# Kernel tuning notes

Measured on AMD Instinct MI355X. Metric: run time of the kernel, lower is better.

## Reference

```python
import jax, jax.numpy as jnp
import numpy as np

N_NODES = 100000
N_EDGES = 1600000
N_REL = 8
IN_CH = 64
HIDDEN = 64
OUT_CH = 32


def setup_inputs() -> dict:
    key = jax.random.key(0)
    ks = jax.random.split(key, 10)
    s_in = 1.0 / np.sqrt(IN_CH)
    s_h = 1.0 / np.sqrt(HIDDEN)
    return {
        "x": jax.random.normal(ks[0], (N_NODES, IN_CH), dtype=jnp.float32),
        "edge_index": jax.random.randint(ks[1], (2, N_EDGES), 0, N_NODES, dtype=jnp.int64),
        "edge_type": jax.random.randint(ks[2], (N_EDGES,), 0, N_REL, dtype=jnp.int64),
        "W0": jax.random.normal(ks[3], (N_REL, IN_CH, HIDDEN), dtype=jnp.float32) * s_in,
        "Q0": jax.random.normal(ks[4], (HIDDEN, 1), dtype=jnp.float32) * s_h,
        "K0": jax.random.normal(ks[5], (HIDDEN, 1), dtype=jnp.float32) * s_h,
        "b0": jnp.zeros((HIDDEN,), dtype=jnp.float32),
        "W1": jax.random.normal(ks[6], (N_REL, HIDDEN, OUT_CH), dtype=jnp.float32) * s_h,
        "Q1": jax.random.normal(ks[7], (OUT_CH, 1), dtype=jnp.float32) * (1.0 / np.sqrt(OUT_CH)),
        "K1": jax.random.normal(ks[8], (OUT_CH, 1), dtype=jnp.float32) * (1.0 / np.sqrt(OUT_CH)),
        "b1": jnp.zeros((OUT_CH,), dtype=jnp.float32),
    }


def rgat_conv(x, src, dst, et, W, Q, K, b, n_nodes):
    # relation-typed transform of all nodes: [R, N, out]
    xw = jnp.einsum("ni,rio->rno", x, W)
    # per-node, per-relation attention logits (heads=1, dim=1)
    q = jnp.einsum("rno,od->rnd", xw, Q)[..., 0]  # [R, N]
    k = jnp.einsum("rno,od->rnd", xw, K)[..., 0]  # [R, N]
    # additive self-attention, leaky_relu slope 0.2 (PyG RGATConv default)
    alpha = jax.nn.leaky_relu(q[et, dst] + k[et, src], negative_slope=0.2)  # [E]
    # across-relation segment softmax over incoming edges of each dst node
    amax = jax.ops.segment_max(alpha, dst, num_segments=n_nodes)
    a = jnp.exp(alpha - amax[dst])
    denom = jax.ops.segment_sum(a, dst, num_segments=n_nodes)
    a = a / (denom[dst] + 1e-16)
    # weighted scatter-add aggregation of transformed source features
    msg = a[:, None] * xw[et, src]  # [E, out]
    return jax.ops.segment_sum(msg, dst, num_segments=n_nodes) + b


def reference(x, edge_index, edge_type, W0, Q0, K0, b0, W1, Q1, K1, b1):
    src, dst = edge_index[0], edge_index[1]
    n = x.shape[0]
    h = rgat_conv(x, src, dst, edge_type, W0, Q0, K0, b0, n)
    h = jax.nn.relu(h)  # dropout p=0.0 -> identity
    out = rgat_conv(h, src, dst, edge_type, W1, Q1, K1, b1, n)
    return out
```

## Files before the change

### kernel.cpp

```cpp
#include <hip/hip_runtime.h>
#include <hip/hip_bf16.h>
#include <math.h>


#define CSR_CHUNK 8192

__global__ void k_bhist(const int* __restrict__ dst, int* __restrict__ bcount,
                        int E, int NB) {
    __shared__ int h[512];
    int t = threadIdx.x;
    for (int i = t; i < NB; i += 256) h[i] = 0;
    __syncthreads();
    int e0 = blockIdx.x * CSR_CHUNK;
    int e1 = min(e0 + CSR_CHUNK, E);
    for (int i = e0 + t; i < e1; i += 256) atomicAdd(&h[dst[i] >> 8], 1);
    __syncthreads();
    for (int i = t; i < NB; i += 256) {
        int c = h[i];
        if (c) atomicAdd(&bcount[i], c);
    }
}

__global__ void k_bscan(const int* __restrict__ bcount, int* __restrict__ bstart,
                        int* __restrict__ gcur, int* __restrict__ rowptr,
                        int NB, int N, int E) {
    __shared__ int s[512];
    int t = threadIdx.x;
    int v = (t < NB) ? bcount[t] : 0;
    s[t] = v;
    __syncthreads();
    for (int off = 1; off < 512; off <<= 1) {
        int a = (t >= off) ? s[t - off] : 0;
        __syncthreads();
        s[t] += a;
        __syncthreads();
    }
    int excl = s[t] - v;
    if (t < NB) {
        bstart[t] = excl;
        gcur[t] = excl;
    }
    if (t == 0) {
        bstart[NB] = E;
        rowptr[N] = E;
    }
}

__global__ void k_bscatter(const int* __restrict__ src, const int* __restrict__ dst,
                           const int* __restrict__ et, int* __restrict__ gcur,
                           unsigned* __restrict__ ebuf, int E, int NB) {
    __shared__ int h[512];
    __shared__ int basearr[512];
    int t = threadIdx.x;
    for (int i = t; i < NB; i += 256) h[i] = 0;
    __syncthreads();
    int e0 = blockIdx.x * CSR_CHUNK;
    int e1 = min(e0 + CSR_CHUNK, E);
    for (int i = e0 + t; i < e1; i += 256) atomicAdd(&h[dst[i] >> 8], 1);
    __syncthreads();
    for (int i = t; i < NB; i += 256) {
        int c = h[i];
        basearr[i] = c ? atomicAdd(&gcur[i], c) : 0;
        h[i] = 0;
    }
    __syncthreads();
    for (int i = e0 + t; i < e1; i += 256) {
        int d = dst[i];
        int b = d >> 8;
        int off = atomicAdd(&h[b], 1);
        ebuf[basearr[b] + off] =
            ((unsigned)(d & 255) << 20) | ((unsigned)et[i] << 17) | (unsigned)src[i];
    }
}

__global__ void k_bsort(const unsigned* __restrict__ ebuf, const int* __restrict__ bstart,
                        int* __restrict__ rowptr, int* __restrict__ csr, int N) {
    __shared__ int lh[2048];
    __shared__ int ls[2048];
    __shared__ int ss[256];
    int b = blockIdx.x, t = threadIdx.x;
    int e0 = bstart[b], e1 = bstart[b + 1];
    for (int i = t; i < 2048; i += 256) lh[i] = 0;
    __syncthreads();
    for (int i = e0 + t; i < e1; i += 256) {
        unsigned u = ebuf[i];
        atomicAdd(&lh[(int)(((u >> 20) & 255) * 8 + ((u >> 17) & 7))], 1);
    }
    __syncthreads();
    int loc[8];
    int s = 0;
#pragma unroll
    for (int j = 0; j < 8; j++) {
        loc[j] = s;
        s += lh[t * 8 + j];
    }
    ss[t] = s;
    __syncthreads();
    for (int off = 1; off < 256; off <<= 1) {
        int a = (t >= off) ? ss[t - off] : 0;
        __syncthreads();
        ss[t] += a;
        __syncthreads();
    }
    int excl = ss[t] - s;
#pragma unroll
    for (int j = 0; j < 8; j++) ls[t * 8 + j] = excl + loc[j];
    int node = b * 256 + t;
    if (node < N) rowptr[node] = e0 + excl;
    __syncthreads();
    for (int i = t; i < 2048; i += 256) lh[i] = 0;
    __syncthreads();
    for (int i = e0 + t; i < e1; i += 256) {
        unsigned u = ebuf[i];
        int key = (int)(((u >> 20) & 255) * 8 + ((u >> 17) & 7));
        int off = atomicAdd(&lh[key], 1);
        csr[e0 + ls[key] + off] = (int)(u & 0xFFFFF);
    }
}


__global__ void k_wt2(const float* __restrict__ W, __hip_bfloat16* __restrict__ hi,
                      __hip_bfloat16* __restrict__ lo, int OUT, int total) {
    int t = blockIdx.x * blockDim.x + threadIdx.x;
    if (t < total) {
        int per = 64 * OUT;
        int r = t / per;
        int rem = t % per;
        int i = rem / OUT;
        int o = rem % OUT;
        float v = W[t];
        __hip_bfloat16 h = __float2bfloat16(v);
        __hip_bfloat16 l = __float2bfloat16(v - __bfloat162float(h));
        size_t idx = (size_t)o * 512 + i * 8 + r;
        hi[idx] = h;
        lo[idx] = l;
    }
}

__global__ void k_wqk(const float* W, const float* Qv, const float* Kv,
                      float* wq, float* wk, int OUT) {
    int t = blockIdx.x * blockDim.x + threadIdx.x;
    if (t < 8 * 64) {
        int r = t >> 6, i = t & 63;
        const float* wrow = W + ((size_t)r * 64 + i) * OUT;
        float a = 0.f, b = 0.f;
        for (int o = 0; o < OUT; o++) {
            float w = wrow[o];
            a += w * Qv[o];
            b += w * Kv[o];
        }
        wq[t] = a;
        wk[t] = b;
    }
}

__global__ __launch_bounds__(256) void k_qk2(
        const float* __restrict__ xin, const float* __restrict__ wq,
        const float* __restrict__ wk, float* __restrict__ qn,
        float* __restrict__ kn, unsigned short* __restrict__ xbb, int N) {
    __shared__ float xt[64][65];
    __shared__ float swq[8 * 65], swk[8 * 65];
    int t = threadIdx.x;
    int nb0 = blockIdx.x * 64;
    for (int i = t; i < 512; i += 256) {
        int r = i >> 6, c = i & 63;
        swq[r * 65 + c] = wq[i];
        swk[r * 65 + c] = wk[i];
    }
    for (int i = t; i < 1024; i += 256) {
        int ns = i >> 4;
        int c4 = i & 15;
        int n = nb0 + ns;
        float4 v = {0.f, 0.f, 0.f, 0.f};
        if (n < N) v = ((const float4*)xin)[(size_t)n * 16 + c4];
        xt[ns][c4 * 4 + 0] = v.x;
        xt[ns][c4 * 4 + 1] = v.y;
        xt[ns][c4 * 4 + 2] = v.z;
        xt[ns][c4 * 4 + 3] = v.w;
        if (n < N) {
            __hip_bfloat16 b0 = __float2bfloat16(v.x);
            __hip_bfloat16 b1 = __float2bfloat16(v.y);
            __hip_bfloat16 b2 = __float2bfloat16(v.z);
            __hip_bfloat16 b3 = __float2bfloat16(v.w);
            ushort4 o;
            o.x = *(unsigned short*)&b0;
            o.y = *(unsigned short*)&b1;
            o.z = *(unsigned short*)&b2;
            o.w = *(unsigned short*)&b3;
            *(ushort4*)(xbb + (size_t)n * 64 + c4 * 4) = o;
        }
    }
    __syncthreads();
#pragma unroll
    for (int g = t; g < 512; g += 256) {
        int ns = g >> 3, r = g & 7;
        int n = nb0 + ns;
        if (n < N) {
            float qa = 0.f, ka = 0.f;
#pragma unroll
            for (int i = 0; i < 64; i++) {
                float xv = xt[ns][i];
                qa += xv * swq[r * 65 + i];
                ka += xv * swk[r * 65 + i];
            }
            qn[(size_t)n * 8 + r] = qa;
            kn[(size_t)n * 8 + r] = ka;
        }
    }
}

__global__ __launch_bounds__(256) void k_agg4(
        const int* __restrict__ rowptr, const int* __restrict__ csr,
        const float* __restrict__ qn, const float* __restrict__ kn,
        const unsigned short* __restrict__ xb,
        __hip_bfloat16* __restrict__ z, int N) {
    int wid = (blockIdx.x * blockDim.x + threadIdx.x) >> 6;
    int lane = threadIdx.x & 63;
    if (wid >= N) return;
    int r0 = rowptr[wid], r1 = rowptr[wid + 1];

    float qv = (lane < 8) ? qn[wid * 8 + lane] : 0.f;

    float denom = 0.f;
    float a0 = 0.f, a1 = 0.f, a2 = 0.f, a3 = 0.f;
    float a4 = 0.f, a5 = 0.f, a6 = 0.f, a7 = 0.f;
    int currel = 0;
    float racc = 0.f;

    for (int base = r0; base < r1; base += 64) {
        int s = base + lane;
        int pk = (s < r1) ? csr[s] : 0;
        int src = pk & 0x1FFFF;
        int rel = pk >> 17;
        float q = __shfl(qv, rel, 64);
        float tv = 0.f;
        if (s < r1) {
            float v = q + kn[src * 8 + rel];
            v = (v >= 0.f) ? v : 0.2f * v;
            tv = __expf(v);
        }
        float ts = tv;
#pragma unroll
        for (int off = 32; off > 0; off >>= 1) ts += __shfl_xor(ts, off, 64);
        denom += ts;

        int cnt = min(64, r1 - base);
        int tvi = (int)__float_as_uint(tv);
        for (int j = 0; j < cnt; j += 16) {
            unsigned p[16];
            float t[16];
#pragma unroll
            for (int u = 0; u < 16; u++) {
                p[u] = (unsigned)__builtin_amdgcn_readlane(pk, j + u);
                t[u] = __uint_as_float((unsigned)__builtin_amdgcn_readlane(tvi, j + u));
            }
            unsigned xu[16];
#pragma unroll
            for (int u = 0; u < 16; u++)
                xu[u] = (unsigned)xb[(size_t)(p[u] & 0x1FFFF) * 64 + lane];
#pragma unroll
            for (int u = 0; u < 16; u++) {
                int rl = (int)(p[u] >> 17);
                if (rl != currel) {
                    switch (currel) {
                        case 0: a0 += racc; break;
                        case 1: a1 += racc; break;
                        case 2: a2 += racc; break;
                        case 3: a3 += racc; break;
                        case 4: a4 += racc; break;
                        case 5: a5 += racc; break;
                        case 6: a6 += racc; break;
                        case 7: a7 += racc; break;
                    }
                    currel = rl;
                    racc = 0.f;
                }
                racc += t[u] * __uint_as_float(xu[u] << 16);
            }
        }
    }
    switch (currel) {
        case 0: a0 += racc; break;
        case 1: a1 += racc; break;
        case 2: a2 += racc; break;
        case 3: a3 += racc; break;
        case 4: a4 += racc; break;
        case 5: a5 += racc; break;
        case 6: a6 += racc; break;
        case 7: a7 += racc; break;
    }

    float inv = 1.f / (denom + 1e-16f);
    unsigned short u[8];
    float av[8] = {a0, a1, a2, a3, a4, a5, a6, a7};
#pragma unroll
    for (int r = 0; r < 8; r++) {
        __hip_bfloat16 b = __float2bfloat16(av[r] * inv);
        u[r] = *(unsigned short*)&b;
    }
    uint4 pack;
    pack.x = (unsigned)u[0] | ((unsigned)u[1] << 16);
    pack.y = (unsigned)u[2] | ((unsigned)u[3] << 16);
    pack.z = (unsigned)u[4] | ((unsigned)u[5] << 16);
    pack.w = (unsigned)u[6] | ((unsigned)u[7] << 16);
    *(uint4*)((unsigned short*)z + (size_t)wid * 512 + lane * 8) = pack;
}

template <int OUT, bool RELU>
__global__ __launch_bounds__(256) void k_zw(
        const __hip_bfloat16* __restrict__ z,
        const __hip_bfloat16* __restrict__ wthi, const __hip_bfloat16* __restrict__ wtlo,
        const float* __restrict__ bias, float* __restrict__ xout, int N) {
    using v8s = __attribute__((ext_vector_type(8))) short;
    using v4f = __attribute__((ext_vector_type(4))) float;
    constexpr int NT = OUT / 16;
    int wave = threadIdx.x >> 6;
    int lane = threadIdx.x & 63;
    int quad = lane >> 4;
    int l15 = lane & 15;
    int m0 = (blockIdx.x * 4 + wave) * 16;
    if (m0 >= N) return;

    const short* zp = (const short*)z;
    const short* wh = (const short*)wthi;
    const short* wl = (const short*)wtlo;
    int n0 = m0 + l15;
    bool valid = n0 < N;

    v8s A[16];
#pragma unroll
    for (int k = 0; k < 16; k++) {
        v8s a = {};
        if (valid) a = *(const v8s*)(zp + (size_t)n0 * 512 + k * 32 + quad * 8);
        A[k] = a;
    }

#pragma unroll
    for (int nt = 0; nt < NT; nt++) {
        const short* bhp = wh + (size_t)(nt * 16 + l15) * 512 + quad * 8;
        const short* blp = wl + (size_t)(nt * 16 + l15) * 512 + quad * 8;
        v4f acc = {0.f, 0.f, 0.f, 0.f};
#pragma unroll
        for (int k = 0; k < 16; k++) {
            v8s bh = *(const v8s*)(bhp + k * 32);
            v8s bl = *(const v8s*)(blp + k * 32);
            acc = __builtin_amdgcn_mfma_f32_16x16x32_bf16(A[k], bh, acc, 0, 0, 0);
            acc = __builtin_amdgcn_mfma_f32_16x16x32_bf16(A[k], bl, acc, 0, 0, 0);
        }
        float bcol = bias[nt * 16 + l15];
#pragma unroll
        for (int g = 0; g < 4; g++) {
            int row = m0 + quad * 4 + g;
            if (row < N) {
                float o = acc[g] + bcol;
                if (RELU) o = fmaxf(o, 0.f);
                xout[(size_t)row * OUT + nt * 16 + l15] = o;
            }
        }
    }
}


extern "C" void kernel_launch(void* const* d_in, const int* in_sizes, int n_in,
                              void* d_out, int out_size, void* d_ws, size_t ws_size,
                              hipStream_t stream) {
    const float* x   = (const float*)d_in[0];
    const int*   ei  = (const int*)d_in[1];
    const int*   et  = (const int*)d_in[2];
    const float* W0  = (const float*)d_in[3];
    const float* Q0  = (const float*)d_in[4];
    const float* K0  = (const float*)d_in[5];
    const float* b0  = (const float*)d_in[6];
    const float* W1  = (const float*)d_in[7];
    const float* Q1  = (const float*)d_in[8];
    const float* K1  = (const float*)d_in[9];
    const float* b1  = (const float*)d_in[10];
    float* out = (float*)d_out;

    const int N = in_sizes[0] / 64;
    const int E = in_sizes[2];
    const int* src = ei;
    const int* dst = ei + E;
    const int NB = (N + 255) >> 8;

    char* p = (char*)d_ws;
    auto alloc = [&](size_t bytes) -> void* {
        void* r = (void*)p;
        p += ((bytes + 255) / 256) * 256;
        return r;
    };
    int* rowptr   = (int*)alloc((size_t)(N + 1) * 4);
    int* bcount   = (int*)alloc(513 * 4);
    int* bstart   = (int*)alloc(513 * 4);
    int* gcur     = (int*)alloc(513 * 4);
    unsigned* ebuf = (unsigned*)alloc((size_t)E * 4);
    int* csr      = (int*)alloc((size_t)E * 4);
    float* wq     = (float*)alloc(8 * 64 * 4);
    float* wk     = (float*)alloc(8 * 64 * 4);
    float* qn     = (float*)alloc((size_t)N * 8 * 4);
    float* kn     = (float*)alloc((size_t)N * 8 * 4);
    __hip_bfloat16* wthi = (__hip_bfloat16*)alloc((size_t)64 * 512 * 2);
    __hip_bfloat16* wtlo = (__hip_bfloat16*)alloc((size_t)64 * 512 * 2);
    __hip_bfloat16* z    = (__hip_bfloat16*)alloc((size_t)N * 512 * 2);
    float* h      = (float*)alloc((size_t)N * 64 * 4);
    unsigned short* xbb = (unsigned short*)alloc((size_t)N * 64 * 2);

    int nchunks = (E + CSR_CHUNK - 1) / CSR_CHUNK;
    hipMemsetAsync(bcount, 0, (size_t)NB * 4, stream);
    k_bhist<<<nchunks, 256, 0, stream>>>(dst, bcount, E, NB);
    k_bscan<<<1, 512, 0, stream>>>(bcount, bstart, gcur, rowptr, NB, N, E);
    k_bscatter<<<nchunks, 256, 0, stream>>>(src, dst, et, gcur, ebuf, E, NB);
    k_bsort<<<NB, 256, 0, stream>>>(ebuf, bstart, rowptr, csr, N);

    int naggb = (N * 64 + 255) / 256;
    int nzwb = (N + 63) / 64;
    int nqkb = (N + 63) / 64;

    k_wqk<<<2, 256, 0, stream>>>(W0, Q0, K0, wq, wk, 64);
    k_qk2<<<nqkb, 256, 0, stream>>>(x, wq, wk, qn, kn, xbb, N);
    k_wt2<<<(8 * 64 * 64 + 255) / 256, 256, 0, stream>>>(W0, wthi, wtlo, 64, 8 * 64 * 64);
    k_agg4<<<naggb, 256, 0, stream>>>(rowptr, csr, qn, kn, xbb, z, N);
    k_zw<64, true><<<nzwb, 256, 0, stream>>>(z, wthi, wtlo, b0, h, N);

    k_wqk<<<2, 256, 0, stream>>>(W1, Q1, K1, wq, wk, 32);
    k_qk2<<<nqkb, 256, 0, stream>>>(h, wq, wk, qn, kn, xbb, N);
    k_wt2<<<(8 * 64 * 32 + 255) / 256, 256, 0, stream>>>(W1, wthi, wtlo, 32, 8 * 64 * 32);
    k_agg4<<<naggb, 256, 0, stream>>>(rowptr, csr, qn, kn, xbb, z, N);
    k_zw<32, false><<<nzwb, 256, 0, stream>>>(z, wthi, wtlo, b1, out, N);
}
```

Baseline: 547.0 us.

## Transform nodes per relation before aggregation instead of aggregating then projecting

Reorders the computation so each layer first computes xw[r,n,:] for all 8 relations with MFMA (split-bf16 precision), then gathers the transformed bf16 rows per edge and accumulates a single channel per lane. This replaces the aggregate-into-per-relation-z (N x 512) then z*W GEMM pipeline and removes the per-relation accumulator switch logic. In exchange it writes and gathers an 8xN x OUT bf16 table, so edge gathers hit relation-scattered rows, and with OUT=32 half the lanes do redundant work.

```diff
diff --git a/kernel.cpp b/kernel.cpp
--- a/kernel.cpp
+++ b/kernel.cpp
@@ -119,8 +119,8 @@
 }
 
 
-__global__ void k_wt2(const float* __restrict__ W, __hip_bfloat16* __restrict__ hi,
-                      __hip_bfloat16* __restrict__ lo, int OUT, int total) {
+__global__ void k_wt(const float* __restrict__ W, __hip_bfloat16* __restrict__ Wthi,
+                     __hip_bfloat16* __restrict__ Wtlo, int OUT, int total) {
     int t = blockIdx.x * blockDim.x + threadIdx.x;
     if (t < total) {
         int per = 64 * OUT;
@@ -129,11 +129,11 @@
         int i = rem / OUT;
         int o = rem % OUT;
         float v = W[t];
-        __hip_bfloat16 h = __float2bfloat16(v);
-        __hip_bfloat16 l = __float2bfloat16(v - __bfloat162float(h));
-        size_t idx = (size_t)o * 512 + i * 8 + r;
-        hi[idx] = h;
-        lo[idx] = l;
+        __hip_bfloat16 hi = __float2bfloat16(v);
+        __hip_bfloat16 lo = __float2bfloat16(v - __bfloat162float(hi));
+        size_t idx = ((size_t)r * OUT + o) * 64 + i;
+        Wthi[idx] = hi;
+        Wtlo[idx] = lo;
     }
 }
 
@@ -157,7 +157,7 @@
 __global__ __launch_bounds__(256) void k_qk2(
         const float* __restrict__ xin, const float* __restrict__ wq,
         const float* __restrict__ wk, float* __restrict__ qn,
-        float* __restrict__ kn, unsigned short* __restrict__ xbb, int N) {
+        float* __restrict__ kn, int N) {
     __shared__ float xt[64][65];
     __shared__ float swq[8 * 65], swk[8 * 65];
     int t = threadIdx.x;
@@ -177,18 +177,6 @@
         xt[ns][c4 * 4 + 1] = v.y;
         xt[ns][c4 * 4 + 2] = v.z;
         xt[ns][c4 * 4 + 3] = v.w;
-        if (n < N) {
-            __hip_bfloat16 b0 = __float2bfloat16(v.x);
-            __hip_bfloat16 b1 = __float2bfloat16(v.y);
-            __hip_bfloat16 b2 = __float2bfloat16(v.z);
-            __hip_bfloat16 b3 = __float2bfloat16(v.w);
-            ushort4 o;
-            o.x = *(unsigned short*)&b0;
-            o.y = *(unsigned short*)&b1;
-            o.z = *(unsigned short*)&b2;
-            o.w = *(unsigned short*)&b3;
-            *(ushort4*)(xbb + (size_t)n * 64 + c4 * 4) = o;
-        }
     }
     __syncthreads();
 #pragma unroll
@@ -209,23 +197,82 @@
     }
 }
 
-__global__ __launch_bounds__(256) void k_agg4(
+template <int OUT>
+__global__ __launch_bounds__(256) void k_xw_mfma(
+        const float* __restrict__ xin,
+        const __hip_bfloat16* __restrict__ wthi, const __hip_bfloat16* __restrict__ wtlo,
+        __hip_bfloat16* __restrict__ xw, int N) {
+    using v8s = __attribute__((ext_vector_type(8))) short;
+    using v4f = __attribute__((ext_vector_type(4))) float;
+    int wave = threadIdx.x >> 6;
+    int lane = threadIdx.x & 63;
+    int quad = lane >> 4;
+    int l15 = lane & 15;
+    int m0 = blockIdx.x * 64 + wave * 16;
+    int node = m0 + l15;
+
+    v8s ahi0 = {}, alo0 = {}, ahi1 = {}, alo1 = {};
+    if (node < N) {
+        const float* xrow = xin + (size_t)node * 64;
+#pragma unroll
+        for (int j = 0; j < 8; j++) {
+            float f0 = xrow[quad * 8 + j];
+            __hip_bfloat16 h0 = __float2bfloat16(f0);
+            __hip_bfloat16 l0 = __float2bfloat16(f0 - __bfloat162float(h0));
+            ahi0[j] = *(short*)&h0;
+            alo0[j] = *(short*)&l0;
+            float f1 = xrow[32 + quad * 8 + j];
+            __hip_bfloat16 h1 = __float2bfloat16(f1);
+            __hip_bfloat16 l1 = __float2bfloat16(f1 - __bfloat162float(h1));
+            ahi1[j] = *(short*)&h1;
+            alo1[j] = *(short*)&l1;
+        }
+    }
+    for (int r = 0; r < 8; r++) {
+        const short* whr = (const short*)(wthi + (size_t)r * OUT * 64);
+        const short* wlr = (const short*)(wtlo + (size_t)r * OUT * 64);
+#pragma unroll
+        for (int nt = 0; nt < OUT; nt += 16) {
+            const short* wh = whr + (nt + l15) * 64;
+            const short* wl = wlr + (nt + l15) * 64;
+            v8s bh0 = *(const v8s*)(wh + quad * 8);
+            v8s bh1 = *(const v8s*)(wh + 32 + quad * 8);
+            v8s bl0 = *(const v8s*)(wl + quad * 8);
+            v8s bl1 = *(const v8s*)(wl + 32 + quad * 8);
+            v4f acc = {0.f, 0.f, 0.f, 0.f};
+            acc = __builtin_amdgcn_mfma_f32_16x16x32_bf16(ahi0, bh0, acc, 0, 0, 0);
+            acc = __builtin_amdgcn_mfma_f32_16x16x32_bf16(ahi1, bh1, acc, 0, 0, 0);
+            acc = __builtin_amdgcn_mfma_f32_16x16x32_bf16(ahi0, bl0, acc, 0, 0, 0);
+            acc = __builtin_amdgcn_mfma_f32_16x16x32_bf16(ahi1, bl1, acc, 0, 0, 0);
+            acc = __builtin_amdgcn_mfma_f32_16x16x32_bf16(alo0, bh0, acc, 0, 0, 0);
+            acc = __builtin_amdgcn_mfma_f32_16x16x32_bf16(alo1, bh1, acc, 0, 0, 0);
+#pragma unroll
+            for (int g = 0; g < 4; g++) {
+                int nrow = m0 + quad * 4 + g;
+                if (nrow < N)
+                    xw[((size_t)r * N + nrow) * OUT + nt + l15] = __float2bfloat16(acc[g]);
+            }
+        }
+    }
+}
+
+template <int OUT, bool RELU>
+__global__ __launch_bounds__(256) void k_agg5(
         const int* __restrict__ rowptr, const int* __restrict__ csr,
         const float* __restrict__ qn, const float* __restrict__ kn,
-        const unsigned short* __restrict__ xb,
-        __hip_bfloat16* __restrict__ z, int N) {
+        const __hip_bfloat16* __restrict__ xw, const float* __restrict__ bias,
+        float* __restrict__ xout, int N) {
     int wid = (blockIdx.x * blockDim.x + threadIdx.x) >> 6;
     int lane = threadIdx.x & 63;
     if (wid >= N) return;
     int r0 = rowptr[wid], r1 = rowptr[wid + 1];
 
     float qv = (lane < 8) ? qn[wid * 8 + lane] : 0.f;
+    int chan = lane & (OUT - 1);
+    const unsigned short* xwp = (const unsigned short*)xw;
 
     float denom = 0.f;
-    float a0 = 0.f, a1 = 0.f, a2 = 0.f, a3 = 0.f;
-    float a4 = 0.f, a5 = 0.f, a6 = 0.f, a7 = 0.f;
-    int currel = 0;
-    float racc = 0.f;
+    float acc = 0.f;
 
     for (int base = r0; base < r1; base += 64) {
         int s = base + lane;
@@ -256,107 +303,21 @@
             }
             unsigned xu[16];
 #pragma unroll
-            for (int u = 0; u < 16; u++)
-                xu[u] = (unsigned)xb[(size_t)(p[u] & 0x1FFFF) * 64 + lane];
-#pragma unroll
             for (int u = 0; u < 16; u++) {
                 int rl = (int)(p[u] >> 17);
-                if (rl != currel) {
-                    switch (currel) {
-                        case 0: a0 += racc; break;
-                        case 1: a1 += racc; break;
-                        case 2: a2 += racc; break;
-                        case 3: a3 += racc; break;
-                        case 4: a4 += racc; break;
-                        case 5: a5 += racc; break;
-                        case 6: a6 += racc; break;
-                        case 7: a7 += racc; break;
-                    }
-                    currel = rl;
-                    racc = 0.f;
-                }
-                racc += t[u] * __uint_as_float(xu[u] << 16);
+                int sr = (int)(p[u] & 0x1FFFF);
+                xu[u] = (unsigned)xwp[((size_t)rl * N + sr) * OUT + chan];
             }
-        }
-    }
-    switch (currel) {
-        case 0: a0 += racc; break;
-        case 1: a1 += racc; break;
-        case 2: a2 += racc; break;
-        case 3: a3 += racc; break;
-        case 4: a4 += racc; break;
-        case 5: a5 += racc; break;
-        case 6: a6 += racc; break;
-        case 7: a7 += racc; break;
-    }
-
-    float inv = 1.f / (denom + 1e-16f);
-    unsigned short u[8];
-    float av[8] = {a0, a1, a2, a3, a4, a5, a6, a7};
-#pragma unroll
-    for (int r = 0; r < 8; r++) {
-        __hip_bfloat16 b = __float2bfloat16(av[r] * inv);
-        u[r] = *(unsigned short*)&b;
-    }
-    uint4 pack;
-    pack.x = (unsigned)u[0] | ((unsigned)u[1] << 16);
-    pack.y = (unsigned)u[2] | ((unsigned)u[3] << 16);
-    pack.z = (unsigned)u[4] | ((unsigned)u[5] << 16);
-    pack.w = (unsigned)u[6] | ((unsigned)u[7] << 16);
-    *(uint4*)((unsigned short*)z + (size_t)wid * 512 + lane * 8) = pack;
-}
-
-template <int OUT, bool RELU>
-__global__ __launch_bounds__(256) void k_zw(
-        const __hip_bfloat16* __restrict__ z,
-        const __hip_bfloat16* __restrict__ wthi, const __hip_bfloat16* __restrict__ wtlo,
-        const float* __restrict__ bias, float* __restrict__ xout, int N) {
-    using v8s = __attribute__((ext_vector_type(8))) short;
-    using v4f = __attribute__((ext_vector_type(4))) float;
-    constexpr int NT = OUT / 16;
-    int wave = threadIdx.x >> 6;
-    int lane = threadIdx.x & 63;
-    int quad = lane >> 4;
-    int l15 = lane & 15;
-    int m0 = (blockIdx.x * 4 + wave) * 16;
-    if (m0 >= N) return;
-
-    const short* zp = (const short*)z;
-    const short* wh = (const short*)wthi;
-    const short* wl = (const short*)wtlo;
-    int n0 = m0 + l15;
-    bool valid = n0 < N;
-
-    v8s A[16];
-#pragma unroll
-    for (int k = 0; k < 16; k++) {
-        v8s a = {};
-        if (valid) a = *(const v8s*)(zp + (size_t)n0 * 512 + k * 32 + quad * 8);
-        A[k] = a;
-    }
-
-#pragma unroll
-    for (int nt = 0; nt < NT; nt++) {
-        const short* bhp = wh + (size_t)(nt * 16 + l15) * 512 + quad * 8;
-        const short* blp = wl + (size_t)(nt * 16 + l15) * 512 + quad * 8;
-        v4f acc = {0.f, 0.f, 0.f, 0.f};
-#pragma unroll
-        for (int k = 0; k < 16; k++) {
-            v8s bh = *(const v8s*)(bhp + k * 32);
-            v8s bl = *(const v8s*)(blp + k * 32);
-            acc = __builtin_amdgcn_mfma_f32_16x16x32_bf16(A[k], bh, acc, 0, 0, 0);
-            acc = __builtin_amdgcn_mfma_f32_16x16x32_bf16(A[k], bl, acc, 0, 0, 0);
-        }
-        float bcol = bias[nt * 16 + l15];
-#pragma unroll
-        for (int g = 0; g < 4; g++) {
-            int row = m0 + quad * 4 + g;
-            if (row < N) {
-                float o = acc[g] + bcol;
-                if (RELU) o = fmaxf(o, 0.f);
-                xout[(size_t)row * OUT + nt * 16 + l15] = o;
-            }
-        }
+#pragma unroll
+            for (int u = 0; u < 16; u++)
+                acc += t[u] * __uint_as_float(xu[u] << 16);
+        }
+    }
+
+    if (lane < OUT) {
+        float o = acc / (denom + 1e-16f) + bias[lane];
+        if (RELU) o = fmaxf(o, 0.f);
+        xout[(size_t)wid * OUT + lane] = o;
     }
 }
 
@@ -399,11 +360,10 @@
     float* wk     = (float*)alloc(8 * 64 * 4);
     float* qn     = (float*)alloc((size_t)N * 8 * 4);
     float* kn     = (float*)alloc((size_t)N * 8 * 4);
-    __hip_bfloat16* wthi = (__hip_bfloat16*)alloc((size_t)64 * 512 * 2);
-    __hip_bfloat16* wtlo = (__hip_bfloat16*)alloc((size_t)64 * 512 * 2);
-    __hip_bfloat16* z    = (__hip_bfloat16*)alloc((size_t)N * 512 * 2);
+    __hip_bfloat16* wthi = (__hip_bfloat16*)alloc((size_t)8 * 64 * 64 * 2);
+    __hip_bfloat16* wtlo = (__hip_bfloat16*)alloc((size_t)8 * 64 * 64 * 2);
+    __hip_bfloat16* xw2  = (__hip_bfloat16*)alloc((size_t)8 * N * 64 * 2);
     float* h      = (float*)alloc((size_t)N * 64 * 4);
-    unsigned short* xbb = (unsigned short*)alloc((size_t)N * 64 * 2);
 
     int nchunks = (E + CSR_CHUNK - 1) / CSR_CHUNK;
     hipMemsetAsync(bcount, 0, (size_t)NB * 4, stream);
@@ -413,18 +373,18 @@
     k_bsort<<<NB, 256, 0, stream>>>(ebuf, bstart, rowptr, csr, N);
 
     int naggb = (N * 64 + 255) / 256;
-    int nzwb = (N + 63) / 64;
+    int nxb = (N + 63) / 64;
     int nqkb = (N + 63) / 64;
 
     k_wqk<<<2, 256, 0, stream>>>(W0, Q0, K0, wq, wk, 64);
-    k_qk2<<<nqkb, 256, 0, stream>>>(x, wq, wk, qn, kn, xbb, N);
-    k_wt2<<<(8 * 64 * 64 + 255) / 256, 256, 0, stream>>>(W0, wthi, wtlo, 64, 8 * 64 * 64);
-    k_agg4<<<naggb, 256, 0, stream>>>(rowptr, csr, qn, kn, xbb, z, N);
-    k_zw<64, true><<<nzwb, 256, 0, stream>>>(z, wthi, wtlo, b0, h, N);
+    k_qk2<<<nqkb, 256, 0, stream>>>(x, wq, wk, qn, kn, N);
+    k_wt<<<(8 * 64 * 64 + 255) / 256, 256, 0, stream>>>(W0, wthi, wtlo, 64, 8 * 64 * 64);
+    k_xw_mfma<64><<<nxb, 256, 0, stream>>>(x, wthi, wtlo, xw2, N);
+    k_agg5<64, true><<<naggb, 256, 0, stream>>>(rowptr, csr, qn, kn, xw2, b0, h, N);
 
     k_wqk<<<2, 256, 0, stream>>>(W1, Q1, K1, wq, wk, 32);
-    k_qk2<<<nqkb, 256, 0, stream>>>(h, wq, wk, qn, kn, xbb, N);
-    k_wt2<<<(8 * 64 * 32 + 255) / 256, 256, 0, stream>>>(W1, wthi, wtlo, 32, 8 * 64 * 32);
-    k_agg4<<<naggb, 256, 0, stream>>>(rowptr, csr, qn, kn, xbb, z, N);
-    k_zw<32, false><<<nzwb, 256, 0, stream>>>(z, wthi, wtlo, b1, out, N);
-}
+    k_qk2<<<nqkb, 256, 0, stream>>>(h, wq, wk, qn, kn, N);
+    k_wt<<<(8 * 64 * 32 + 255) / 256, 256, 0, stream>>>(W1, wthi, wtlo, 32, 8 * 64 * 32);
+    k_xw_mfma<32><<<nxb, 256, 0, stream>>>(h, wthi, wtlo, xw2, N);
+    k_agg5<32, false><<<naggb, 256, 0, stream>>>(rowptr, csr, qn, kn, xw2, b1, out, N);
+}
```

After: 505.7 us. 7.5% less time.
